# Kernel optimization log

Measured on AMD Instinct MI355X. Metric: run time of the kernel, lower is better.

The kernel has to match this reference:

```python
import jax, jax.numpy as jnp
import numpy as np

NUM_HEADS = 8
WINDOW = 5


def local_mask(T, w):
    # non-causal band: attend iff |i - j| <= w
    i = jnp.arange(T)
    return jnp.abs(i[:, None] - i[None, :]) <= w


def setup_inputs() -> dict:
    key = jax.random.key(0)
    k1, k2, k3 = jax.random.split(key, 3)
    B, T, S, C = 2, 64, 1024, 512  # batch, frames, spatial (32x32), hidden
    x = jax.random.normal(k1, (B, T * S, C), dtype=jnp.float32)
    W_qkv = jax.random.normal(k2, (C, 3 * C), dtype=jnp.float32) * (C ** -0.5)
    W_out = jax.random.normal(k3, (C, C), dtype=jnp.float32) * (C ** -0.5)
    return {"x": x, "W_qkv": W_qkv, "W_out": W_out, "num_frames": T}


def reference(x, W_qkv, W_out, num_frames):
    B, N, C = x.shape
    H = NUM_HEADS
    hd = C // H
    T = num_frames
    S = N // T
    scale = hd ** -0.5

    qkv = (x @ W_qkv).reshape(B, T, S, 3, H, hd)
    q = qkv[:, :, :, 0]  # [B,T,S,H,hd]
    k = qkv[:, :, :, 1]
    v = qkv[:, :, :, 2]

    # temporal attention: independent per (batch, head, spatial location)
    scores = jnp.einsum('btshd,bushd->bhstu', q, k) * scale  # [B,H,S,T,T]
    mask = local_mask(T, WINDOW)  # [T,T]
    scores = jnp.where(mask[None, None, None], scores, -jnp.inf)
    attn = jax.nn.softmax(scores, axis=-1)
    out = jnp.einsum('bhstu,bushd->btshd', attn, v)  # [B,T,S,H,hd]
    out = out.reshape(B, N, C) @ W_out
    return out
```

## Files before the change

### kernel.cpp

```cpp
#include <hip/hip_runtime.h>
#include <stdint.h>

#define B_   2
#define T_   64
#define S_   1024
#define C_   512
#define H_   8
#define N_   (T_ * S_)
#define M_   (B_ * N_)
#define WIN_ 5

typedef unsigned short u16;
typedef __bf16 bf16;
typedef __bf16 bf16x8 __attribute__((ext_vector_type(8)));
typedef float  f32x4  __attribute__((ext_vector_type(4)));
typedef u16    u16x8  __attribute__((ext_vector_type(8)));

static __device__ __forceinline__ u16 f2bf(float f) {
    return __builtin_bit_cast(u16, (bf16)f);
}
static __device__ __forceinline__ float bf2f(u16 u) {
    return __builtin_bit_cast(float, (uint32_t)u << 16);
}
static __device__ __forceinline__ void gload16(const void* g, void* l) {
    __builtin_amdgcn_global_load_lds(
        (const __attribute__((address_space(1))) void*)g,
        (__attribute__((address_space(3))) void*)l, 16, 0, 0);
}
static __device__ __forceinline__ long permute_row(long grow) {
    int b = (int)(grow >> 16);
    int t = (int)(grow >> 10) & 63;
    int s = (int)grow & 1023;
    return ((long)((b << 10) | s)) * 64 + t;
}


__global__ __launch_bounds__(256) void prep_w(const float* __restrict__ W,
                                              u16* __restrict__ WT, int NCOL) {
    int id = blockIdx.x * 256 + threadIdx.x;
    int n  = id % NCOL;
    int gi = id / NCOL;
    int chunk = gi >> 2;
    int g     = gi & 3;
    int k0 = chunk * 32 + g * 8;
    int cs = chunk ^ ((n >> 3) & 1);
    int gs = g ^ ((n >> 1) & 3);
    u16x8 w;
    #pragma unroll
    for (int j = 0; j < 8; ++j) w[j] = f2bf(W[(size_t)(k0 + j) * NCOL + n]);
    *(u16x8*)&WT[(size_t)n * 512 + cs * 32 + gs * 8] = w;
}

__global__ __launch_bounds__(256) void prep_w2(const float* __restrict__ W,
                                               u16* __restrict__ WT2) {
    int id = blockIdx.x * 256 + threadIdx.x;
    int n  = id % 1536;
    int gi = id / 1536;
    int chunk = gi >> 2;
    int g     = gi & 3;
    int k0 = chunk * 32 + g * 8;
    int which = n >> 9;
    int h     = (n >> 6) & 7;
    int d     = n & 63;
    int rloc  = which * 64 + d;
    long np   = h * 192 + rloc;
    int cs = chunk ^ ((rloc >> 3) & 1);
    int gs = g ^ ((rloc >> 1) & 3);
    u16x8 w;
    #pragma unroll
    for (int j = 0; j < 8; ++j) w[j] = f2bf(W[(size_t)(k0 + j) * 1536 + n]);
    *(u16x8*)&WT2[(size_t)np * 512 + cs * 32 + gs * 8] = w;
}

__global__ __launch_bounds__(256) void prep_x(const float* __restrict__ x,
                                              u16* __restrict__ xb) {
    const size_t total = (size_t)M_ * 64;
    for (size_t id = (size_t)blockIdx.x * 256 + threadIdx.x; id < total;
         id += (size_t)gridDim.x * 256) {
        long r_in = (long)(id >> 6);
        int  gi   = (int)(id & 63);
        int chunk = gi >> 2;
        int g     = gi & 3;
        long rid  = permute_row(r_in);
        int cb  = (int)(rid >> 3) & 1;
        int key = (int)(rid >> 1) & 3;
        const float* src = x + r_in * 512 + chunk * 32 + g * 8;
        f32x4 v0 = *(const f32x4*)(src);
        f32x4 v1 = *(const f32x4*)(src + 4);
        u16x8 w;
        #pragma unroll
        for (int j = 0; j < 4; ++j) { w[j] = f2bf(v0[j]); w[4 + j] = f2bf(v1[j]); }
        *(u16x8*)&xb[(size_t)rid * 512 + (chunk ^ cb) * 32 + ((g ^ key) << 3)] = w;
    }
}

#define LDF(off) __builtin_bit_cast(bf16x8, *(const u16x8*)&lds[(off)])
#define MFMA16(d, a, b) d = __builtin_amdgcn_mfma_f32_16x16x32_bf16(a, b, d, 0, 0, 0)

#define PSTR 200

__global__ __launch_bounds__(512, 4) void gemm_attn(const u16* __restrict__ Ap,
                                                    const u16* __restrict__ Bp,
                                                    u16* __restrict__ attn) {
    __shared__ u16 lds[40960];

    const int tid  = threadIdx.x;
    const int lane = tid & 63;
    const int wid  = tid >> 6;
    const int wm   = wid >> 2;
    const int wn   = wid & 3;
    const int fr   = lane & 15;
    const int g0   = lane >> 4;

    const int rowtile = ((blockIdx.x >> 6) << 3) | (blockIdx.x & 7);
    const int h       = (blockIdx.x >> 3) & 7;
    const long row0   = (long)rowtile * 128;

    int aoffs[4], boffs[3];
    #pragma unroll
    for (int mf = 0; mf < 4; ++mf) {
        int lr = wm * 64 + mf * 16 + fr;
        aoffs[mf] = lr * 64 + (((lr >> 3) & 1) << 5) + (((g0 ^ (lr >> 1)) & 3) << 3);
    }
    #pragma unroll
    for (int nf = 0; nf < 3; ++nf) {
        int lc = wn * 48 + nf * 16 + fr;
        boffs[nf] = lc * 64 + (((lc >> 3) & 1) << 5) + (((g0 ^ (lc >> 1)) & 3) << 3);
    }

    const int srow = lane >> 3;
    const int scol = (lane & 7) * 8;

    auto stageA = [&](int tt, int half) {
        const int ab = (tt & 1) * 8192;
        int r = half * 64 + wid * 8 + srow;
        const u16* g = Ap + (row0 + r) * 512 + tt * 64 + scol;
        gload16(g, (void*)&lds[ab + r * 64]);
    };
    auto stageB = [&](int tt) {
        const int bb = 16384 + (tt & 1) * 12288;
        #pragma unroll
        for (int i = 0; i < 3; ++i) {
            int r = i * 64 + wid * 8 + srow;
            const u16* g = Bp + (size_t)(h * 192 + r) * 512 + tt * 64 + scol;
            gload16(g, (void*)&lds[bb + r * 64]);
        }
    };

    f32x4 acc[4][3] = {};

    stageA(0, 0); stageA(0, 1); stageB(0); stageB(1);
    asm volatile("s_waitcnt vmcnt(3)" ::: "memory");
    __builtin_amdgcn_sched_barrier(0);
    __builtin_amdgcn_s_barrier();

    #pragma unroll
    for (int t = 0; t < 8; ++t) {
        const int ab = (t & 1) * 8192;
        const int bb = 16384 + (t & 1) * 12288;
        bf16x8 af[4], bfv[3];
        #pragma unroll
        for (int mf = 0; mf < 4; ++mf) af[mf] = LDF(ab + aoffs[mf]);
        #pragma unroll
        for (int nf = 0; nf < 3; ++nf) bfv[nf] = LDF(bb + boffs[nf]);
        if (t <= 6) { stageA(t + 1, 0); stageA(t + 1, 1); }
        __builtin_amdgcn_s_barrier();
        asm volatile("s_waitcnt lgkmcnt(0)" ::: "memory");
        __builtin_amdgcn_sched_barrier(0);
        __builtin_amdgcn_s_setprio(1);
        #pragma unroll
        for (int mf = 0; mf < 4; ++mf) {
            MFMA16(acc[mf][0], af[mf], bfv[0]);
            MFMA16(acc[mf][1], af[mf], bfv[1]);
            MFMA16(acc[mf][2], af[mf], bfv[2]);
        }
        __builtin_amdgcn_s_setprio(0);
        __builtin_amdgcn_s_barrier();
        #pragma unroll
        for (int mf = 0; mf < 4; ++mf) af[mf] = LDF(ab + (aoffs[mf] ^ 32));
        #pragma unroll
        for (int nf = 0; nf < 3; ++nf) bfv[nf] = LDF(bb + (boffs[nf] ^ 32));
        __builtin_amdgcn_s_barrier();
        asm volatile("s_waitcnt lgkmcnt(0)" ::: "memory");
        __builtin_amdgcn_sched_barrier(0);
        __builtin_amdgcn_s_setprio(1);
        #pragma unroll
        for (int mf = 0; mf < 4; ++mf) {
            MFMA16(acc[mf][0], af[mf], bfv[0]);
            MFMA16(acc[mf][1], af[mf], bfv[1]);
            MFMA16(acc[mf][2], af[mf], bfv[2]);
        }
        __builtin_amdgcn_s_setprio(0);
        __builtin_amdgcn_s_barrier();
        if (t <= 6) {
            if (t <= 5) {
                stageB(t + 2);
                asm volatile("s_waitcnt vmcnt(3)" ::: "memory");
            } else {
                asm volatile("s_waitcnt vmcnt(0)" ::: "memory");
            }
            __builtin_amdgcn_sched_barrier(0);
            __builtin_amdgcn_s_barrier();
        }
    }

    __builtin_amdgcn_sched_barrier(0);
    #pragma unroll
    for (int mf = 0; mf < 4; ++mf) {
        #pragma unroll
        for (int nf = 0; nf < 3; ++nf) {
            #pragma unroll
            for (int r = 0; r < 4; ++r) {
                int row = wm * 64 + mf * 16 + (lane >> 4) * 4 + r;
                int col = wn * 48 + nf * 16 + fr;
                lds[row * PSTR + col] = f2bf(acc[mf][nf][r]);
            }
        }
    }
    __syncthreads();

    if (wid < 2) {
        const int slab = wid;
        const int t = lane;
        const int prow = slab * 64 + t;
        float qf[64];
        #pragma unroll
        for (int c = 0; c < 8; ++c) {
            u16x8 v = *(const u16x8*)&lds[prow * PSTR + c * 8];
            #pragma unroll
            for (int j = 0; j < 8; ++j) qf[c * 8 + j] = bf2f(v[j]);
        }
        float p[11];
        float m = -1e30f;
        #pragma unroll
        for (int i = 0; i < 11; ++i) {
            int u = t - WIN_ + i;
            if (u >= 0 && u < 64) {
                const int ub = (slab * 64 + u) * PSTR + 64;
                float dot = 0.f;
                #pragma unroll
                for (int c = 0; c < 8; ++c) {
                    u16x8 kv = *(const u16x8*)&lds[ub + c * 8];
                    #pragma unroll
                    for (int j = 0; j < 8; ++j) dot += qf[c * 8 + j] * bf2f(kv[j]);
                }
                p[i] = dot * 0.125f;
                m = fmaxf(m, p[i]);
            } else {
                p[i] = -1e30f;
            }
        }
        float sum = 0.f;
        #pragma unroll
        for (int i = 0; i < 11; ++i) {
            int u = t - WIN_ + i;
            float e = (u >= 0 && u < 64) ? __expf(p[i] - m) : 0.f;
            p[i] = e;
            sum += e;
        }
        const float inv = 1.f / sum;
        float o[64];
        #pragma unroll
        for (int d = 0; d < 64; ++d) o[d] = 0.f;
        #pragma unroll
        for (int i = 0; i < 11; ++i) {
            int u = t - WIN_ + i;
            if (u >= 0 && u < 64) {
                const int ub = (slab * 64 + u) * PSTR + 128;
                float pv = p[i] * inv;
                #pragma unroll
                for (int c = 0; c < 8; ++c) {
                    u16x8 vv = *(const u16x8*)&lds[ub + c * 8];
                    #pragma unroll
                    for (int j = 0; j < 8; ++j) o[c * 8 + j] += pv * bf2f(vv[j]);
                }
            }
        }
        long rid = row0 + prow;
        int s = (int)(rid >> 6) & 1023;
        size_t rowbase = (size_t)rid * C_;
        const int cb  = (s >> 3) & 1;
        const int key = (s >> 1) & 3;
        #pragma unroll
        for (int c = 0; c < 8; ++c) {
            u16x8 w;
            #pragma unroll
            for (int j = 0; j < 8; ++j) w[j] = f2bf(o[c * 8 + j]);
            int off = (((2 * h + (c >> 2)) ^ cb) << 5) + (((c & 3) ^ key) << 3);
            *(u16x8*)&attn[rowbase + off] = w;
        }
    }
}

template<int NCOL, bool OUT_BF16, bool A_PERM>
__global__ __launch_bounds__(512, 2) void gemm8_k(const u16* __restrict__ Ap,
                                                  const u16* __restrict__ Bp,
                                                  void* __restrict__ Dp, int gx) {
    __shared__ u16 lds[65536];

    const int tid  = threadIdx.x;
    const int lane = tid & 63;
    const int wid  = tid >> 6;
    const int wm   = wid >> 2;
    const int wn   = wid & 3;
    const int fr   = lane & 15;
    const int g0   = lane >> 4;

    const int nwg = gridDim.x;
    const int q8  = nwg >> 3;
    const int bid = blockIdx.x;
    const int wg  = (bid & 7) * q8 + (bid >> 3);
    const int bx  = wg % gx;
    const int by  = wg / gx;
    const long row0 = (long)by * 256;
    const int  col0 = bx * 256;

    int aoffs[8], boffs[4];
    #pragma unroll
    for (int mf = 0; mf < 8; ++mf) {
        int lr = wm * 128 + mf * 16 + fr;
        aoffs[mf] = lr * 64 + (((lr >> 3) & 1) << 5) + (((g0 ^ (lr >> 1)) & 3) << 3);
    }
    #pragma unroll
    for (int nf = 0; nf < 4; ++nf) {
        int lc = wn * 64 + nf * 16 + fr;
        boffs[nf] = lc * 64 + (((lc >> 3) & 1) << 5) + (((g0 ^ (lc >> 1)) & 3) << 3);
    }

    const int srow = lane >> 3;
    const int scol = (lane & 7) * 8;

    long arow_phys[4];
    #pragma unroll
    for (int half = 0; half < 2; ++half)
        #pragma unroll
        for (int i = 0; i < 2; ++i) {
            int r = half * 128 + i * 64 + wid * 8 + srow;
            long grow = row0 + r;
            arow_phys[half * 2 + i] = A_PERM ? permute_row(grow) : grow;
        }

    auto stageA = [&](int tt, int half) {
        const int ab = (tt & 1) * 32768;
        #pragma unroll
        for (int i = 0; i < 2; ++i) {
            int r = half * 128 + i * 64 + wid * 8 + srow;
            const u16* g = Ap + arow_phys[half * 2 + i] * 512 + tt * 64 + scol;
            gload16(g, (void*)&lds[ab + r * 64]);
        }
    };
    auto stageB = [&](int tt, int half) {
        const int ab = (tt & 1) * 32768;
        #pragma unroll
        for (int i = 0; i < 2; ++i) {
            int r = half * 128 + i * 64 + wid * 8 + srow;
            const u16* g = Bp + (size_t)(col0 + r) * 512 + tt * 64 + scol;
            gload16(g, (void*)&lds[ab + 16384 + r * 64]);
        }
    };

    f32x4 acc[8][4] = {};

    stageA(0, 0); stageA(0, 1); stageB(0, 0); stageB(0, 1);
    stageB(1, 0); stageB(1, 1);
    asm volatile("s_waitcnt vmcnt(4)" ::: "memory");
    __builtin_amdgcn_sched_barrier(0);
    __builtin_amdgcn_s_barrier();

    #pragma unroll
    for (int t = 0; t < 8; ++t) {
        const int ab = (t & 1) * 32768;
        bf16x8 af0[8], af1[8], bf0[4], bf1[4];
        #pragma unroll
        for (int mf = 0; mf < 4; ++mf) af0[mf] = LDF(ab + aoffs[mf]);
        #pragma unroll
        for (int nf = 0; nf < 4; ++nf) bf0[nf] = LDF(ab + 16384 + boffs[nf]);
        if (t <= 6) stageA(t + 1, 0);
        __builtin_amdgcn_s_barrier();
        asm volatile("s_waitcnt lgkmcnt(0)" ::: "memory");
        __builtin_amdgcn_sched_barrier(0);
        __builtin_amdgcn_s_setprio(1);
        #pragma unroll
        for (int mf = 0; mf < 4; ++mf) {
            MFMA16(acc[mf][0], af0[mf], bf0[0]);
            MFMA16(acc[mf][1], af0[mf], bf0[1]);
            MFMA16(acc[mf][2], af0[mf], bf0[2]);
            MFMA16(acc[mf][3], af0[mf], bf0[3]);
        }
        __builtin_amdgcn_s_setprio(0);
        __builtin_amdgcn_s_barrier();
        #pragma unroll
        for (int mf = 4; mf < 8; ++mf) af0[mf] = LDF(ab + aoffs[mf]);
        #pragma unroll
        for (int nf = 0; nf < 4; ++nf) bf1[nf] = LDF(ab + 16384 + (boffs[nf] ^ 32));
        if (t <= 6) stageA(t + 1, 1);
        __builtin_amdgcn_s_barrier();
        asm volatile("s_waitcnt lgkmcnt(0)" ::: "memory");
        __builtin_amdgcn_sched_barrier(0);
        __builtin_amdgcn_s_setprio(1);
        #pragma unroll
        for (int mf = 4; mf < 8; ++mf) {
            MFMA16(acc[mf][0], af0[mf], bf0[0]);
            MFMA16(acc[mf][1], af0[mf], bf0[1]);
            MFMA16(acc[mf][2], af0[mf], bf0[2]);
            MFMA16(acc[mf][3], af0[mf], bf0[3]);
        }
        __builtin_amdgcn_s_setprio(0);
        __builtin_amdgcn_s_barrier();
        #pragma unroll
        for (int mf = 0; mf < 4; ++mf) af1[mf] = LDF(ab + (aoffs[mf] ^ 32));
        if (t <= 5) stageB(t + 2, 0);
        __builtin_amdgcn_s_barrier();
        asm volatile("s_waitcnt lgkmcnt(0)" ::: "memory");
        __builtin_amdgcn_sched_barrier(0);
        __builtin_amdgcn_s_setprio(1);
        #pragma unroll
        for (int mf = 0; mf < 4; ++mf) {
            MFMA16(acc[mf][0], af1[mf], bf1[0]);
            MFMA16(acc[mf][1], af1[mf], bf1[1]);
            MFMA16(acc[mf][2], af1[mf], bf1[2]);
            MFMA16(acc[mf][3], af1[mf], bf1[3]);
        }
        __builtin_amdgcn_s_setprio(0);
        __builtin_amdgcn_s_barrier();
        #pragma unroll
        for (int mf = 4; mf < 8; ++mf) af1[mf] = LDF(ab + (aoffs[mf] ^ 32));
        if (t <= 5) stageB(t + 2, 1);
        __builtin_amdgcn_s_barrier();
        asm volatile("s_waitcnt lgkmcnt(0)" ::: "memory");
        __builtin_amdgcn_sched_barrier(0);
        __builtin_amdgcn_s_setprio(1);
        #pragma unroll
        for (int mf = 4; mf < 8; ++mf) {
            MFMA16(acc[mf][0], af1[mf], bf1[0]);
            MFMA16(acc[mf][1], af1[mf], bf1[1]);
            MFMA16(acc[mf][2], af1[mf], bf1[2]);
            MFMA16(acc[mf][3], af1[mf], bf1[3]);
        }
        __builtin_amdgcn_s_setprio(0);
        if (t <= 5) {
            asm volatile("s_waitcnt vmcnt(4)" ::: "memory");
        } else if (t == 6) {
            asm volatile("s_waitcnt vmcnt(0)" ::: "memory");
        }
        __builtin_amdgcn_sched_barrier(0);
        __builtin_amdgcn_s_barrier();
    }

    #pragma unroll
    for (int mf = 0; mf < 8; ++mf) {
        #pragma unroll
        for (int nf = 0; nf < 4; ++nf) {
            #pragma unroll
            for (int r = 0; r < 4; ++r) {
                long grow = row0 + wm * 128 + mf * 16 + (lane >> 4) * 4 + r;
                int  gcol = col0 + wn * 64 + nf * 16 + fr;
                float v = acc[mf][nf][r];
                if constexpr (OUT_BF16) ((u16*)Dp)[grow * NCOL + gcol] = f2bf(v);
                else                    ((float*)Dp)[grow * NCOL + gcol] = v;
            }
        }
    }
}

extern "C" void kernel_launch(void* const* d_in, const int* in_sizes, int n_in,
                              void* d_out, int out_size, void* d_ws, size_t ws_size,
                              hipStream_t stream) {
    const float* x    = (const float*)d_in[0];
    const float* Wqkv = (const float*)d_in[1];
    const float* Wout = (const float*)d_in[2];
    float* out = (float*)d_out;

    const size_t xc_elems = (size_t)M_ * C_;
    u16* xb       = (u16*)d_ws;
    u16* attn_buf = xb + xc_elems;
    u16* WqkvT2   = attn_buf + xc_elems;
    u16* WoutT    = WqkvT2 + (size_t)1536 * 512;
    if (ws_size < ((size_t)(WoutT + (size_t)512 * 512) - (size_t)d_ws)) return;

    prep_w2<<<(1536 * 64) / 256, 256, 0, stream>>>(Wqkv, WqkvT2);
    prep_w<<<(512 * 64) / 256, 256, 0, stream>>>(Wout, WoutT, 512);
    prep_x<<<8192, 256, 0, stream>>>(x, xb);

    gemm_attn<<<8192, 512, 0, stream>>>(xb, WqkvT2, attn_buf);

    gemm8_k<512, false, true><<<1024, 512, 0, stream>>>(attn_buf, WoutT, (void*)out, 2);
}
```

Measured before the change: 510.6 us.

## Split local attention epilogue across all eight waves by head-dim quarters

The fused QKV+attention epilogue previously ran on only two of eight waves, each lane computing full 64-dim dot products and outputs. Now all eight waves participate: each wave handles one slab and a 16-dim quarter of the head dimension, writes partial QK dot products to an LDS scratch area, synchronizes, then sums the partials for the softmax. This cuts the serial tail and register pressure of the epilogue, at the cost of an extra barrier, LDS scratch traffic, and softmax work repeated in each wave.

```diff
diff --git a/kernel.cpp b/kernel.cpp
--- a/kernel.cpp
+++ b/kernel.cpp
@@ -219,32 +219,45 @@
     }
     __syncthreads();
 
-    if (wid < 2) {
-        const int slab = wid;
-        const int t = lane;
+    {
+        const int slab = wid >> 2;
+        const int q    = wid & 3;
+        const int t    = lane;
         const int prow = slab * 64 + t;
-        float qf[64];
-        #pragma unroll
-        for (int c = 0; c < 8; ++c) {
-            u16x8 v = *(const u16x8*)&lds[prow * PSTR + c * 8];
+        float* scr = (float*)&lds[25600];
+
+        float qf[16];
+        #pragma unroll
+        for (int cc = 0; cc < 2; ++cc) {
+            u16x8 v = *(const u16x8*)&lds[prow * PSTR + (q * 2 + cc) * 8];
             #pragma unroll
-            for (int j = 0; j < 8; ++j) qf[c * 8 + j] = bf2f(v[j]);
-        }
+            for (int j = 0; j < 8; ++j) qf[cc * 8 + j] = bf2f(v[j]);
+        }
+        #pragma unroll
+        for (int i = 0; i < 11; ++i) {
+            int u = t - WIN_ + i;
+            float dot = 0.f;
+            if (u >= 0 && u < 64) {
+                const int ub = (slab * 64 + u) * PSTR + 64;
+                #pragma unroll
+                for (int cc = 0; cc < 2; ++cc) {
+                    u16x8 kv = *(const u16x8*)&lds[ub + (q * 2 + cc) * 8];
+                    #pragma unroll
+                    for (int j = 0; j < 8; ++j) dot += qf[cc * 8 + j] * bf2f(kv[j]);
+                }
+            }
+            scr[(prow * 11 + i) * 4 + q] = dot;
+        }
+        __syncthreads();
+
         float p[11];
         float m = -1e30f;
         #pragma unroll
         for (int i = 0; i < 11; ++i) {
             int u = t - WIN_ + i;
             if (u >= 0 && u < 64) {
-                const int ub = (slab * 64 + u) * PSTR + 64;
-                float dot = 0.f;
-                #pragma unroll
-                for (int c = 0; c < 8; ++c) {
-                    u16x8 kv = *(const u16x8*)&lds[ub + c * 8];
-                    #pragma unroll
-                    for (int j = 0; j < 8; ++j) dot += qf[c * 8 + j] * bf2f(kv[j]);
-                }
-                p[i] = dot * 0.125f;
+                f32x4 v = *(const f32x4*)&scr[(prow * 11 + i) * 4];
+                p[i] = (v[0] + v[1] + v[2] + v[3]) * 0.125f;
                 m = fmaxf(m, p[i]);
             } else {
                 p[i] = -1e30f;
@@ -259,9 +272,10 @@
             sum += e;
         }
         const float inv = 1.f / sum;
-        float o[64];
-        #pragma unroll
-        for (int d = 0; d < 64; ++d) o[d] = 0.f;
+
+        float o[16];
+        #pragma unroll
+        for (int d = 0; d < 16; ++d) o[d] = 0.f;
         #pragma unroll
         for (int i = 0; i < 11; ++i) {
             int u = t - WIN_ + i;
@@ -269,10 +283,10 @@
                 const int ub = (slab * 64 + u) * PSTR + 128;
                 float pv = p[i] * inv;
                 #pragma unroll
-                for (int c = 0; c < 8; ++c) {
-                    u16x8 vv = *(const u16x8*)&lds[ub + c * 8];
+                for (int cc = 0; cc < 2; ++cc) {
+                    u16x8 vv = *(const u16x8*)&lds[ub + (q * 2 + cc) * 8];
                     #pragma unroll
-                    for (int j = 0; j < 8; ++j) o[c * 8 + j] += pv * bf2f(vv[j]);
+                    for (int j = 0; j < 8; ++j) o[cc * 8 + j] += pv * bf2f(vv[j]);
                 }
             }
         }
@@ -282,10 +296,11 @@
         const int cb  = (s >> 3) & 1;
         const int key = (s >> 1) & 3;
         #pragma unroll
-        for (int c = 0; c < 8; ++c) {
+        for (int cc = 0; cc < 2; ++cc) {
+            int c = q * 2 + cc;
             u16x8 w;
             #pragma unroll
-            for (int j = 0; j < 8; ++j) w[j] = f2bf(o[c * 8 + j]);
+            for (int j = 0; j < 8; ++j) w[j] = f2bf(o[cc * 8 + j]);
             int off = (((2 * h + (c >> 2)) ^ cb) << 5) + (((c & 3) ^ key) << 3);
             *(u16x8*)&attn[rowbase + off] = w;
         }
```

Result: faster. 485.4 us (-4.9%).
